# Performance work log

Measured on AMD Instinct MI355X. Metric: run time of the kernel, lower is better.

## Reference

```python
import jax, jax.numpy as jnp
import numpy as np

B, T, D, H = 32, 2048, 256, 256

def setup_inputs() -> dict:
    key = jax.random.key(0)
    ks = jax.random.split(key, 5)
    s = 1.0 / np.sqrt(H)  # PyTorch default uniform scale
    return {
        "x": jax.random.normal(ks[0], (B, T, D), dtype=jnp.float32),
        "W_ih": jax.random.uniform(ks[1], (4 * H, D), jnp.float32, -s, s),
        "W_hh": jax.random.uniform(ks[2], (4 * H, H), jnp.float32, -s, s),
        "b_ih": jax.random.uniform(ks[3], (4 * H,), jnp.float32, -s, s),
        "b_hh": jax.random.uniform(ks[4], (4 * H,), jnp.float32, -s, s),
    }

def reference(x, W_ih, W_hh, b_ih, b_hh):
    # x: [B,T,D]. relu then single-layer LSTM (PyTorch gate order i,f,g,o).
    xr = jax.nn.relu(x)
    # Precompute input contribution to gates: [B,T,4H] -> scan over T as [T,B,4H]
    xg = jnp.einsum("btd,gd->btg", xr, W_ih) + b_ih + b_hh
    xg = jnp.transpose(xg, (1, 0, 2))
    W_hh_T = W_hh.T  # [H,4H]

    def step(carry, xt):
        h, c = carry
        gates = xt + h @ W_hh_T  # [B,4H]
        i, f, g, o = jnp.split(gates, 4, axis=-1)
        i = jax.nn.sigmoid(i)
        f = jax.nn.sigmoid(f)
        g = jnp.tanh(g)
        o = jax.nn.sigmoid(o)
        c = f * c + i * g
        h = o * jnp.tanh(c)
        return (h, c), h

    h0 = jnp.zeros((B, H), dtype=x.dtype)
    c0 = jnp.zeros((B, H), dtype=x.dtype)
    _, ys = jax.lax.scan(step, (h0, c0), xg)  # ys: [T,B,H]
    # dropout p=0.0 (eval) -> identity
    return jnp.transpose(ys, (1, 0, 2))  # [B,T,H]
```

## Files before the change

kernel.cpp:

```cpp
#include <hip/hip_runtime.h>


#define T_STEPS 2048
#define DDIM 256
#define HDIM 256
#define GROUPS 2
#define PARTS 8
#define NBLOCKS (GROUPS * PARTS)
#define NTHREADS 512

typedef __attribute__((ext_vector_type(8))) short short8;
typedef __attribute__((ext_vector_type(4))) float float4_;
typedef __attribute__((ext_vector_type(2))) float float2_;

__device__ inline unsigned short f2bf(float f) {
    unsigned u = __float_as_uint(f);
    return (unsigned short)((u + 0x7fffu + ((u >> 16) & 1u)) >> 16);
}
__device__ inline float sigmoid_f(float x) { return 1.f / (1.f + __expf(-x)); }
__device__ inline float tanh_f(float x) { return 1.f - 2.f / (__expf(2.f * x) + 1.f); }

__global__ __launch_bounds__(NTHREADS, 2)
void lstm_persistent(const float* __restrict__ x,
                     const float* __restrict__ Wih,
                     const float* __restrict__ Whh,
                     const float* __restrict__ bih,
                     const float* __restrict__ bhh,
                     float* __restrict__ out,
                     unsigned int* __restrict__ hbuf,
                     int* __restrict__ flags)
{
    const int tid  = threadIdx.x;
    const int blk  = blockIdx.x;
    const int g    = blk >> 3;
    const int p    = blk & 7;
    const int w    = tid >> 6;
    const int lane = tid & 63;
    const int c16  = lane & 15;
    const int quad = lane >> 4;

    __shared__ float gatesLds[128 * 17];
    __shared__ float biasLds[128];

    if (tid < 128) {
        int n = ((tid >> 5) << 8) + (p << 5) + (tid & 31);
        biasLds[tid] = bih[n] + bhh[n];
    }

    const int r_row = (w << 4) + c16;
    const int wrow  = ((r_row >> 5) << 8) + (p << 5) + (r_row & 31);
    const int k0    = quad << 3;

    short8 wih_f[8], whh_f[8];
#pragma unroll
    for (int kt = 0; kt < 8; ++kt) {
        const float* s1 = Wih + wrow * DDIM + kt * 32 + k0;
        const float* s2 = Whh + wrow * HDIM + kt * 32 + k0;
        short8 v1, v2;
#pragma unroll
        for (int j = 0; j < 8; ++j) { v1[j] = (short)f2bf(s1[j]); v2[j] = (short)f2bf(s2[j]); }
        wih_f[kt] = v1;
        whh_f[kt] = v2;
    }

    const float* xlane = x + (size_t)(g * 16 + c16) * (size_t)(T_STEPS * DDIM);
    float4_ xraw[16];
#pragma unroll
    for (int kt = 0; kt < 8; ++kt) {
        const float* sx = xlane + kt * 32 + k0;
        xraw[2 * kt]     = *(const float4_*)(sx);
        xraw[2 * kt + 1] = *(const float4_*)(sx + 4);
    }

    const int b_e = tid & 15;
    const int up  = (tid >> 4) & 15;
    float c0 = 0.f, c1 = 0.f;

    const int myflag = blk << 4;

    for (int s = 0; s < T_STEPS; ++s) {
        short8 xf[8];
#pragma unroll
        for (int kt = 0; kt < 8; ++kt) {
            short8 v;
#pragma unroll
            for (int j = 0; j < 4; ++j) {
                float a = xraw[2 * kt][j];
                float b = xraw[2 * kt + 1][j];
                v[j]     = (short)f2bf(a > 0.f ? a : 0.f);
                v[j + 4] = (short)f2bf(b > 0.f ? b : 0.f);
            }
            xf[kt] = v;
        }
        float4_ acc0 = {0.f, 0.f, 0.f, 0.f};
        float4_ acc1 = {0.f, 0.f, 0.f, 0.f};
#pragma unroll
        for (int kt = 0; kt < 8; kt += 2) {
            acc0 = __builtin_amdgcn_mfma_f32_16x16x32_bf16(xf[kt],     wih_f[kt],     acc0, 0, 0, 0);
            acc1 = __builtin_amdgcn_mfma_f32_16x16x32_bf16(xf[kt + 1], wih_f[kt + 1], acc1, 0, 0, 0);
        }
        {
            int sn = (s + 1 < T_STEPS) ? s + 1 : s;
            const float* sx = xlane + (size_t)sn * DDIM + k0;
#pragma unroll
            for (int kt = 0; kt < 8; ++kt) {
                xraw[2 * kt]     = *(const float4_*)(sx + kt * 32);
                xraw[2 * kt + 1] = *(const float4_*)(sx + kt * 32 + 4);
            }
        }

        if (tid < PARTS) {
            const int* fp = flags + ((g * PARTS + tid) << 4);
            while (__hip_atomic_load(fp, __ATOMIC_RELAXED, __HIP_MEMORY_SCOPE_AGENT) < s) { }
        }
        __syncthreads();

        const unsigned long long* hq = (const unsigned long long*)
            ((const char*)hbuf + (size_t)(((g * 2 + (s & 1)) * 16 + c16) * 512) + (size_t)(k0 * 2));
        short8 hf[8];
#pragma unroll
        for (int kt = 0; kt < 8; ++kt) {
            unsigned long long q0 = __hip_atomic_load(hq + kt * 8,     __ATOMIC_RELAXED, __HIP_MEMORY_SCOPE_AGENT);
            unsigned long long q1 = __hip_atomic_load(hq + kt * 8 + 1, __ATOMIC_RELAXED, __HIP_MEMORY_SCOPE_AGENT);
            union { unsigned long long q[2]; short8 v; } cvt;
            cvt.q[0] = q0; cvt.q[1] = q1;
            hf[kt] = cvt.v;
        }

#pragma unroll
        for (int kt = 0; kt < 8; kt += 2) {
            acc0 = __builtin_amdgcn_mfma_f32_16x16x32_bf16(hf[kt],     whh_f[kt],     acc0, 0, 0, 0);
            acc1 = __builtin_amdgcn_mfma_f32_16x16x32_bf16(hf[kt + 1], whh_f[kt + 1], acc1, 0, 0, 0);
        }

#pragma unroll
        for (int j = 0; j < 4; ++j)
            gatesLds[r_row * 17 + (quad << 2) + j] = acc0[j] + acc1[j];
        __syncthreads();

        if (tid < 256) {
            const int u0 = up << 1, u1 = (up << 1) + 1;
            float gi0 = gatesLds[u0 * 17 + b_e]         + biasLds[u0];
            float gf0 = gatesLds[(32 + u0) * 17 + b_e]  + biasLds[32 + u0];
            float gg0 = gatesLds[(64 + u0) * 17 + b_e]  + biasLds[64 + u0];
            float go0 = gatesLds[(96 + u0) * 17 + b_e]  + biasLds[96 + u0];
            float gi1 = gatesLds[u1 * 17 + b_e]         + biasLds[u1];
            float gf1 = gatesLds[(32 + u1) * 17 + b_e]  + biasLds[32 + u1];
            float gg1 = gatesLds[(64 + u1) * 17 + b_e]  + biasLds[64 + u1];
            float go1 = gatesLds[(96 + u1) * 17 + b_e]  + biasLds[96 + u1];

            c0 = sigmoid_f(gf0) * c0 + sigmoid_f(gi0) * tanh_f(gg0);
            c1 = sigmoid_f(gf1) * c1 + sigmoid_f(gi1) * tanh_f(gg1);
            float h0 = sigmoid_f(go0) * tanh_f(c0);
            float h1 = sigmoid_f(go1) * tanh_f(c1);

            unsigned hv = (unsigned)f2bf(h0) | ((unsigned)f2bf(h1) << 16);
            unsigned int* hd = hbuf + (((g * 2 + ((s + 1) & 1)) * 16 + b_e) << 7) + (p << 4) + up;
            __hip_atomic_store(hd, hv, __ATOMIC_RELAXED, __HIP_MEMORY_SCOPE_AGENT);

            float2_ ov = {h0, h1};
            *(float2_*)(out + ((size_t)(g * 16 + b_e) * T_STEPS + (size_t)s) * HDIM + (p << 5) + u0) = ov;
        }

        __builtin_amdgcn_s_waitcnt(0);
        __syncthreads();
        if (tid == 0)
            __hip_atomic_store(flags + myflag, s + 1,
                               __ATOMIC_RELAXED, __HIP_MEMORY_SCOPE_AGENT);
    }
}

extern "C" void kernel_launch(void* const* d_in, const int* in_sizes, int n_in,
                              void* d_out, int out_size, void* d_ws, size_t ws_size,
                              hipStream_t stream) {
    (void)in_sizes; (void)n_in; (void)out_size; (void)ws_size;
    const float* x   = (const float*)d_in[0];
    const float* Wih = (const float*)d_in[1];
    const float* Whh = (const float*)d_in[2];
    const float* bih = (const float*)d_in[3];
    const float* bhh = (const float*)d_in[4];
    float* out = (float*)d_out;

    unsigned int* hbuf = (unsigned int*)d_ws;
    int* flags         = (int*)((char*)d_ws + 32768);

    hipMemsetAsync(d_ws, 0, 32768 + NBLOCKS * 64, stream);
    hipLaunchKernelGGL(lstm_persistent, dim3(NBLOCKS), dim3(NTHREADS), 0, stream,
                       x, Wih, Whh, bih, bhh, out, hbuf, flags);
}
```

Baseline: 18.16 ms.

## Replace per-block flag barrier with step-tagged hidden-state words

Each packed bf16 hidden pair now carries the producer's step number in the upper 32 bits of a 64-bit word. Consumers spin directly on the data until every word they read has the expected tag. This removes the separate flag array, the waitcnt, the end-of-step syncthreads and the flag store. The MFMA accumulation is also split across four independent accumulators to shorten dependency chains. The cost is twice the hidden-state traffic, since each read is 64 bits instead of 32, and wavefronts may re-poll many words while they wait.

```diff
diff --git a/kernel.cpp b/kernel.cpp
--- a/kernel.cpp
+++ b/kernel.cpp
@@ -27,8 +27,7 @@
                      const float* __restrict__ bih,
                      const float* __restrict__ bhh,
                      float* __restrict__ out,
-                     unsigned int* __restrict__ hbuf,
-                     int* __restrict__ flags)
+                     unsigned long long* __restrict__ hbuf)
 {
     const int tid  = threadIdx.x;
     const int blk  = blockIdx.x;
@@ -76,8 +75,6 @@
     const int up  = (tid >> 4) & 15;
     float c0 = 0.f, c1 = 0.f;
 
-    const int myflag = blk << 4;
-
     for (int s = 0; s < T_STEPS; ++s) {
         short8 xf[8];
 #pragma unroll
@@ -92,13 +89,13 @@
             }
             xf[kt] = v;
         }
-        float4_ acc0 = {0.f, 0.f, 0.f, 0.f};
-        float4_ acc1 = {0.f, 0.f, 0.f, 0.f};
+        float4_ acc[4];
 #pragma unroll
-        for (int kt = 0; kt < 8; kt += 2) {
-            acc0 = __builtin_amdgcn_mfma_f32_16x16x32_bf16(xf[kt],     wih_f[kt],     acc0, 0, 0, 0);
-            acc1 = __builtin_amdgcn_mfma_f32_16x16x32_bf16(xf[kt + 1], wih_f[kt + 1], acc1, 0, 0, 0);
-        }
+        for (int i = 0; i < 4; ++i) acc[i] = (float4_){0.f, 0.f, 0.f, 0.f};
+#pragma unroll
+        for (int kt = 0; kt < 8; ++kt)
+            acc[kt & 3] = __builtin_amdgcn_mfma_f32_16x16x32_bf16(xf[kt], wih_f[kt], acc[kt & 3], 0, 0, 0);
+
         {
             int sn = (s + 1 < T_STEPS) ? s + 1 : s;
             const float* sx = xlane + (size_t)sn * DDIM + k0;
@@ -109,45 +106,55 @@
             }
         }
 
-        if (tid < PARTS) {
-            const int* fp = flags + ((g * PARTS + tid) << 4);
-            while (__hip_atomic_load(fp, __ATOMIC_RELAXED, __HIP_MEMORY_SCOPE_AGENT) < s) { }
-        }
-        __syncthreads();
-
-        const unsigned long long* hq = (const unsigned long long*)
-            ((const char*)hbuf + (size_t)(((g * 2 + (s & 1)) * 16 + c16) * 512) + (size_t)(k0 * 2));
         short8 hf[8];
+        {
+            const unsigned tag = (unsigned)s;
+            const unsigned long long* hq =
+                hbuf + (size_t)(((g * 2 + (s & 1)) * 16 + c16) * 128 + quad * 4);
+            for (;;) {
+                unsigned long long q[32];
 #pragma unroll
-        for (int kt = 0; kt < 8; ++kt) {
-            unsigned long long q0 = __hip_atomic_load(hq + kt * 8,     __ATOMIC_RELAXED, __HIP_MEMORY_SCOPE_AGENT);
-            unsigned long long q1 = __hip_atomic_load(hq + kt * 8 + 1, __ATOMIC_RELAXED, __HIP_MEMORY_SCOPE_AGENT);
-            union { unsigned long long q[2]; short8 v; } cvt;
-            cvt.q[0] = q0; cvt.q[1] = q1;
-            hf[kt] = cvt.v;
+                for (int kt = 0; kt < 8; ++kt)
+#pragma unroll
+                    for (int i = 0; i < 4; ++i)
+                        q[4 * kt + i] = __hip_atomic_load(hq + kt * 16 + i,
+                                            __ATOMIC_RELAXED, __HIP_MEMORY_SCOPE_AGENT);
+                unsigned chk = 0;
+#pragma unroll
+                for (int i = 0; i < 32; ++i) chk |= (unsigned)(q[i] >> 32) ^ tag;
+                if (!__any(chk != 0)) {
+#pragma unroll
+                    for (int kt = 0; kt < 8; ++kt) {
+                        union { unsigned u[4]; short8 v; } cv;
+#pragma unroll
+                        for (int i = 0; i < 4; ++i) cv.u[i] = (unsigned)q[4 * kt + i];
+                        hf[kt] = cv.v;
+                    }
+                    break;
+                }
+            }
         }
 
 #pragma unroll
-        for (int kt = 0; kt < 8; kt += 2) {
-            acc0 = __builtin_amdgcn_mfma_f32_16x16x32_bf16(hf[kt],     whh_f[kt],     acc0, 0, 0, 0);
-            acc1 = __builtin_amdgcn_mfma_f32_16x16x32_bf16(hf[kt + 1], whh_f[kt + 1], acc1, 0, 0, 0);
-        }
+        for (int kt = 0; kt < 8; ++kt)
+            acc[kt & 3] = __builtin_amdgcn_mfma_f32_16x16x32_bf16(hf[kt], whh_f[kt], acc[kt & 3], 0, 0, 0);
 
 #pragma unroll
         for (int j = 0; j < 4; ++j)
-            gatesLds[r_row * 17 + (quad << 2) + j] = acc0[j] + acc1[j];
+            gatesLds[r_row * 17 + (quad << 2) + j] =
+                (acc[0][j] + acc[1][j]) + (acc[2][j] + acc[3][j]);
         __syncthreads();
 
         if (tid < 256) {
-            const int u0 = up << 1, u1 = (up << 1) + 1;
-            float gi0 = gatesLds[u0 * 17 + b_e]         + biasLds[u0];
-            float gf0 = gatesLds[(32 + u0) * 17 + b_e]  + biasLds[32 + u0];
-            float gg0 = gatesLds[(64 + u0) * 17 + b_e]  + biasLds[64 + u0];
-            float go0 = gatesLds[(96 + u0) * 17 + b_e]  + biasLds[96 + u0];
-            float gi1 = gatesLds[u1 * 17 + b_e]         + biasLds[u1];
-            float gf1 = gatesLds[(32 + u1) * 17 + b_e]  + biasLds[32 + u1];
-            float gg1 = gatesLds[(64 + u1) * 17 + b_e]  + biasLds[64 + u1];
-            float go1 = gatesLds[(96 + u1) * 17 + b_e]  + biasLds[96 + u1];
+            const int u0 = up << 1, u1 = u0 + 1;
+            float gi0 = gatesLds[u0 * 17 + b_e]        + biasLds[u0];
+            float gf0 = gatesLds[(32 + u0) * 17 + b_e] + biasLds[32 + u0];
+            float gg0 = gatesLds[(64 + u0) * 17 + b_e] + biasLds[64 + u0];
+            float go0 = gatesLds[(96 + u0) * 17 + b_e] + biasLds[96 + u0];
+            float gi1 = gatesLds[u1 * 17 + b_e]        + biasLds[u1];
+            float gf1 = gatesLds[(32 + u1) * 17 + b_e] + biasLds[32 + u1];
+            float gg1 = gatesLds[(64 + u1) * 17 + b_e] + biasLds[64 + u1];
+            float go1 = gatesLds[(96 + u1) * 17 + b_e] + biasLds[96 + u1];
 
             c0 = sigmoid_f(gf0) * c0 + sigmoid_f(gi0) * tanh_f(gg0);
             c1 = sigmoid_f(gf1) * c1 + sigmoid_f(gi1) * tanh_f(gg1);
@@ -155,18 +162,15 @@
             float h1 = sigmoid_f(go1) * tanh_f(c1);
 
             unsigned hv = (unsigned)f2bf(h0) | ((unsigned)f2bf(h1) << 16);
-            unsigned int* hd = hbuf + (((g * 2 + ((s + 1) & 1)) * 16 + b_e) << 7) + (p << 4) + up;
-            __hip_atomic_store(hd, hv, __ATOMIC_RELAXED, __HIP_MEMORY_SCOPE_AGENT);
+            unsigned long long word = (unsigned long long)hv
+                                    | ((unsigned long long)(unsigned)(s + 1) << 32);
+            unsigned long long* hd =
+                hbuf + (size_t)(((g * 2 + ((s + 1) & 1)) * 16 + b_e) * 128 + p * 16 + up);
+            __hip_atomic_store(hd, word, __ATOMIC_RELAXED, __HIP_MEMORY_SCOPE_AGENT);
 
             float2_ ov = {h0, h1};
             *(float2_*)(out + ((size_t)(g * 16 + b_e) * T_STEPS + (size_t)s) * HDIM + (p << 5) + u0) = ov;
         }
-
-        __builtin_amdgcn_s_waitcnt(0);
-        __syncthreads();
-        if (tid == 0)
-            __hip_atomic_store(flags + myflag, s + 1,
-                               __ATOMIC_RELAXED, __HIP_MEMORY_SCOPE_AGENT);
     }
 }
 
@@ -181,10 +185,9 @@
     const float* bhh = (const float*)d_in[4];
     float* out = (float*)d_out;
 
-    unsigned int* hbuf = (unsigned int*)d_ws;
-    int* flags         = (int*)((char*)d_ws + 32768);
+    unsigned long long* hbuf = (unsigned long long*)d_ws;
 
-    hipMemsetAsync(d_ws, 0, 32768 + NBLOCKS * 64, stream);
+    hipMemsetAsync(d_ws, 0, 65536, stream);
     hipLaunchKernelGGL(lstm_persistent, dim3(NBLOCKS), dim3(NTHREADS), 0, stream,
-                       x, Wih, Whh, bih, bhh, out, hbuf, flags);
+                       x, Wih, Whh, bih, bhh, out, hbuf);
 }
```

After: 24.27 ms. 33.6% more time.

## Co-locate group blocks on one XCD and use sc0 L2-coherent flag sync

Applied to the files above, without the earlier changes.

The grid grows to 64 blocks and keeps only those whose block index mod 8 is below GROUPS, so that under round-robin XCD dispatch each group's 8 blocks likely share one XCD and its L2. A runtime probe checks this by having the blocks exchange tokens with sc0 loads and stores; if every block sees the tokens within a bound, the group switches to a cheaper protocol. That protocol uses per-wave atomic-add counters, sc0 loads for h, double-buffered gate LDS, and drops the trailing barrier and flag store. The aim is to cut the per-step cross-block synchronization latency that dominates this latency-bound recurrence. The cost is extra idle blocks, a probe at startup, and reliance on a dispatch-placement assumption, with a fallback to the original path when the probe fails.

```diff
diff --git a/kernel.cpp b/kernel.cpp
--- a/kernel.cpp
+++ b/kernel.cpp
@@ -6,12 +6,17 @@
 #define HDIM 256
 #define GROUPS 2
 #define PARTS 8
-#define NBLOCKS (GROUPS * PARTS)
 #define NTHREADS 512
+#define GRID 64
+
+#define PROBE_ROUNDS 6
+#define PROBE_BOUND_FIRST 30000
+#define PROBE_BOUND_LATER 3000
 
 typedef __attribute__((ext_vector_type(8))) short short8;
 typedef __attribute__((ext_vector_type(4))) float float4_;
 typedef __attribute__((ext_vector_type(2))) float float2_;
+typedef __attribute__((ext_vector_type(4))) unsigned uint4_;
 
 __device__ inline unsigned short f2bf(float f) {
     unsigned u = __float_as_uint(f);
@@ -19,6 +24,191 @@
 }
 __device__ inline float sigmoid_f(float x) { return 1.f / (1.f + __expf(-x)); }
 __device__ inline float tanh_f(float x) { return 1.f - 2.f / (__expf(2.f * x) + 1.f); }
+
+__device__ __forceinline__ unsigned ld_u32_sc0(const unsigned* p) {
+    unsigned v;
+    asm volatile("global_load_dword %0, %1, off sc0\n\ts_waitcnt vmcnt(0)"
+                 : "=&v"(v) : "v"(p) : "memory");
+    return v;
+}
+__device__ __forceinline__ void st_u32_sc0(unsigned* p, unsigned v) {
+    asm volatile("global_store_dword %0, %1, off sc0" :: "v"(p), "v"(v) : "memory");
+}
+__device__ __forceinline__ void atomic_add_u32(unsigned* p, unsigned v) {
+    asm volatile("global_atomic_add %0, %1, off" :: "v"(p), "v"(v) : "memory");
+}
+__device__ __forceinline__ unsigned ldmin8_sc0(const unsigned* p) {
+    unsigned a0,a1,a2,a3,a4,a5,a6,a7;
+    asm volatile(
+        "global_load_dword %0, %8, off sc0\n\t"
+        "global_load_dword %1, %8, off offset:64 sc0\n\t"
+        "global_load_dword %2, %8, off offset:128 sc0\n\t"
+        "global_load_dword %3, %8, off offset:192 sc0\n\t"
+        "global_load_dword %4, %8, off offset:256 sc0\n\t"
+        "global_load_dword %5, %8, off offset:320 sc0\n\t"
+        "global_load_dword %6, %8, off offset:384 sc0\n\t"
+        "global_load_dword %7, %8, off offset:448 sc0\n\t"
+        "s_waitcnt vmcnt(0)"
+        : "=&v"(a0), "=&v"(a1), "=&v"(a2), "=&v"(a3),
+          "=&v"(a4), "=&v"(a5), "=&v"(a6), "=&v"(a7)
+        : "v"(p) : "memory");
+    unsigned m = a0 < a1 ? a0 : a1;
+    m = a2 < m ? a2 : m;  m = a3 < m ? a3 : m;
+    m = a4 < m ? a4 : m;  m = a5 < m ? a5 : m;
+    m = a6 < m ? a6 : m;  m = a7 < m ? a7 : m;
+    return m;
+}
+__device__ __forceinline__ void ld_hrow_sc0(const char* p, short8 hf[8]) {
+    uint4_ a0, a1, a2, a3, a4, a5, a6, a7;
+    asm volatile(
+        "global_load_dwordx4 %0, %8, off sc0\n\t"
+        "global_load_dwordx4 %1, %8, off offset:64 sc0\n\t"
+        "global_load_dwordx4 %2, %8, off offset:128 sc0\n\t"
+        "global_load_dwordx4 %3, %8, off offset:192 sc0\n\t"
+        "global_load_dwordx4 %4, %8, off offset:256 sc0\n\t"
+        "global_load_dwordx4 %5, %8, off offset:320 sc0\n\t"
+        "global_load_dwordx4 %6, %8, off offset:384 sc0\n\t"
+        "global_load_dwordx4 %7, %8, off offset:448 sc0\n\t"
+        "s_waitcnt vmcnt(0)"
+        : "=&v"(a0), "=&v"(a1), "=&v"(a2), "=&v"(a3),
+          "=&v"(a4), "=&v"(a5), "=&v"(a6), "=&v"(a7)
+        : "v"(p) : "memory");
+    union { uint4_ u; short8 s; } c;
+    c.u = a0; hf[0] = c.s;  c.u = a1; hf[1] = c.s;
+    c.u = a2; hf[2] = c.s;  c.u = a3; hf[3] = c.s;
+    c.u = a4; hf[4] = c.s;  c.u = a5; hf[5] = c.s;
+    c.u = a6; hf[6] = c.s;  c.u = a7; hf[7] = c.s;
+}
+
+template<bool COLOC>
+__device__ __forceinline__ void lstm_loop(
+    const float* __restrict__ xlane, float* __restrict__ out,
+    char* __restrict__ hbase, unsigned* __restrict__ flags,
+    float (*gatesLds)[128 * 17], const float* biasLds,
+    short8* wih_f, short8* whh_f, float4_* xraw,
+    int g, int p, int tid, int lane, int c16, int quad, int r_row)
+{
+    const int b_e = tid & 15;
+    const int up  = (tid >> 4) & 15;
+    const int k0  = quad << 3;
+    float c0 = 0.f, c1 = 0.f;
+
+    for (int s = 0; s < T_STEPS; ++s) {
+        float* gates = COLOC ? gatesLds[s & 1] : gatesLds[0];
+
+        short8 xf[8];
+#pragma unroll
+        for (int kt = 0; kt < 8; ++kt) {
+            short8 v;
+#pragma unroll
+            for (int j = 0; j < 4; ++j) {
+                float a = xraw[2 * kt][j];
+                float b = xraw[2 * kt + 1][j];
+                v[j]     = (short)f2bf(a > 0.f ? a : 0.f);
+                v[j + 4] = (short)f2bf(b > 0.f ? b : 0.f);
+            }
+            xf[kt] = v;
+        }
+        float4_ acc[4];
+#pragma unroll
+        for (int i = 0; i < 4; ++i) acc[i] = (float4_){0.f, 0.f, 0.f, 0.f};
+#pragma unroll
+        for (int kt = 0; kt < 8; ++kt)
+            acc[kt & 3] = __builtin_amdgcn_mfma_f32_16x16x32_bf16(xf[kt], wih_f[kt], acc[kt & 3], 0, 0, 0);
+
+        {
+            int sn = (s + 1 < T_STEPS) ? s + 1 : s;
+            const float* sx = xlane + (size_t)sn * DDIM + k0;
+#pragma unroll
+            for (int kt = 0; kt < 8; ++kt) {
+                xraw[2 * kt]     = *(const float4_*)(sx + kt * 32);
+                xraw[2 * kt + 1] = *(const float4_*)(sx + kt * 32 + 4);
+            }
+        }
+
+        if (COLOC) {
+            const unsigned thr = 4u * (unsigned)s;
+            if (lane < PARTS) {
+                const unsigned* cp = flags + (size_t)(g * PARTS + lane) * 16;
+                while (ld_u32_sc0(cp) < thr) { }
+            }
+        } else {
+            if (tid < PARTS) {
+                const int* fp = (const int*)(flags + (size_t)(g * PARTS + tid) * 16);
+                while (__hip_atomic_load(fp, __ATOMIC_RELAXED, __HIP_MEMORY_SCOPE_AGENT) < s) { }
+            }
+            __syncthreads();
+        }
+
+        short8 hf[8];
+        const char* hb = hbase + (size_t)(((g * 2 + (s & 1)) * 16 + c16) * 512 + quad * 16);
+        if (COLOC) {
+            ld_hrow_sc0(hb, hf);
+        } else {
+            const unsigned long long* hq = (const unsigned long long*)hb;
+#pragma unroll
+            for (int kt = 0; kt < 8; ++kt) {
+                unsigned long long q0 = __hip_atomic_load(hq + kt * 8,     __ATOMIC_RELAXED, __HIP_MEMORY_SCOPE_AGENT);
+                unsigned long long q1 = __hip_atomic_load(hq + kt * 8 + 1, __ATOMIC_RELAXED, __HIP_MEMORY_SCOPE_AGENT);
+                union { unsigned long long q[2]; short8 v; } cvt;
+                cvt.q[0] = q0; cvt.q[1] = q1;
+                hf[kt] = cvt.v;
+            }
+        }
+
+#pragma unroll
+        for (int kt = 0; kt < 8; ++kt)
+            acc[kt & 3] = __builtin_amdgcn_mfma_f32_16x16x32_bf16(hf[kt], whh_f[kt], acc[kt & 3], 0, 0, 0);
+
+#pragma unroll
+        for (int j = 0; j < 4; ++j)
+            gates[r_row * 17 + (quad << 2) + j] =
+                (acc[0][j] + acc[1][j]) + (acc[2][j] + acc[3][j]);
+        __syncthreads();
+
+        if (tid < 256) {
+            const int u0 = up << 1, u1 = u0 + 1;
+            float gi0 = gates[u0 * 17 + b_e]        + biasLds[u0];
+            float gf0 = gates[(32 + u0) * 17 + b_e] + biasLds[32 + u0];
+            float gg0 = gates[(64 + u0) * 17 + b_e] + biasLds[64 + u0];
+            float go0 = gates[(96 + u0) * 17 + b_e] + biasLds[96 + u0];
+            float gi1 = gates[u1 * 17 + b_e]        + biasLds[u1];
+            float gf1 = gates[(32 + u1) * 17 + b_e] + biasLds[32 + u1];
+            float gg1 = gates[(64 + u1) * 17 + b_e] + biasLds[64 + u1];
+            float go1 = gates[(96 + u1) * 17 + b_e] + biasLds[96 + u1];
+
+            c0 = sigmoid_f(gf0) * c0 + sigmoid_f(gi0) * tanh_f(gg0);
+            c1 = sigmoid_f(gf1) * c1 + sigmoid_f(gi1) * tanh_f(gg1);
+            float h0 = sigmoid_f(go0) * tanh_f(c0);
+            float h1 = sigmoid_f(go1) * tanh_f(c1);
+
+            unsigned hv = (unsigned)f2bf(h0) | ((unsigned)f2bf(h1) << 16);
+            unsigned* hd = (unsigned*)(hbase +
+                (size_t)(((g * 2 + ((s + 1) & 1)) * 16 + b_e) * 512 + (p * 16 + up) * 4));
+
+            if (COLOC) {
+                st_u32_sc0(hd, hv);
+                asm volatile("s_waitcnt vmcnt(0)" ::: "memory");
+                if ((tid & 63) == 0)
+                    atomic_add_u32(flags + (size_t)(g * PARTS + p) * 16, 1u);
+                float2_ ov = {h0, h1};
+                *(float2_*)(out + ((size_t)(g * 16 + b_e) * T_STEPS + (size_t)s) * HDIM + (p << 5) + u0) = ov;
+            } else {
+                __hip_atomic_store(hd, hv, __ATOMIC_RELAXED, __HIP_MEMORY_SCOPE_AGENT);
+                float2_ ov = {h0, h1};
+                *(float2_*)(out + ((size_t)(g * 16 + b_e) * T_STEPS + (size_t)s) * HDIM + (p << 5) + u0) = ov;
+            }
+        }
+
+        if (!COLOC) {
+            __builtin_amdgcn_s_waitcnt(0);
+            __syncthreads();
+            if (tid == 0)
+                __hip_atomic_store((int*)(flags + (size_t)(g * PARTS + p) * 16), s + 1,
+                                   __ATOMIC_RELAXED, __HIP_MEMORY_SCOPE_AGENT);
+        }
+    }
+}
 
 __global__ __launch_bounds__(NTHREADS, 2)
 void lstm_persistent(const float* __restrict__ x,
@@ -27,20 +217,25 @@
                      const float* __restrict__ bih,
                      const float* __restrict__ bhh,
                      float* __restrict__ out,
-                     unsigned int* __restrict__ hbuf,
-                     int* __restrict__ flags)
+                     char* __restrict__ hbase,
+                     unsigned* __restrict__ flags,
+                     unsigned* __restrict__ probe,
+                     unsigned* __restrict__ votes,
+                     unsigned* __restrict__ verdict)
 {
-    const int tid  = threadIdx.x;
-    const int blk  = blockIdx.x;
-    const int g    = blk >> 3;
-    const int p    = blk & 7;
+    const int tid = threadIdx.x;
+    const int blk = blockIdx.x;
+    if ((blk & 7) >= GROUPS) return;
+    const int g = blk & 7;
+    const int p = blk >> 3;
     const int w    = tid >> 6;
     const int lane = tid & 63;
     const int c16  = lane & 15;
     const int quad = lane >> 4;
 
-    __shared__ float gatesLds[128 * 17];
+    __shared__ float gatesLds[2][128 * 17];
     __shared__ float biasLds[128];
+    __shared__ int colocSh;
 
     if (tid < 128) {
         int n = ((tid >> 5) << 8) + (p << 5) + (tid & 31);
@@ -72,102 +267,50 @@
         xraw[2 * kt + 1] = *(const float4_*)(sx + 4);
     }
 
-    const int b_e = tid & 15;
-    const int up  = (tid >> 4) & 15;
-    float c0 = 0.f, c1 = 0.f;
-
-    const int myflag = blk << 4;
-
-    for (int s = 0; s < T_STEPS; ++s) {
-        short8 xf[8];
-#pragma unroll
-        for (int kt = 0; kt < 8; ++kt) {
-            short8 v;
-#pragma unroll
-            for (int j = 0; j < 4; ++j) {
-                float a = xraw[2 * kt][j];
-                float b = xraw[2 * kt + 1][j];
-                v[j]     = (short)f2bf(a > 0.f ? a : 0.f);
-                v[j + 4] = (short)f2bf(b > 0.f ? b : 0.f);
-            }
-            xf[kt] = v;
-        }
-        float4_ acc0 = {0.f, 0.f, 0.f, 0.f};
-        float4_ acc1 = {0.f, 0.f, 0.f, 0.f};
-#pragma unroll
-        for (int kt = 0; kt < 8; kt += 2) {
-            acc0 = __builtin_amdgcn_mfma_f32_16x16x32_bf16(xf[kt],     wih_f[kt],     acc0, 0, 0, 0);
-            acc1 = __builtin_amdgcn_mfma_f32_16x16x32_bf16(xf[kt + 1], wih_f[kt + 1], acc1, 0, 0, 0);
-        }
-        {
-            int sn = (s + 1 < T_STEPS) ? s + 1 : s;
-            const float* sx = xlane + (size_t)sn * DDIM + k0;
-#pragma unroll
-            for (int kt = 0; kt < 8; ++kt) {
-                xraw[2 * kt]     = *(const float4_*)(sx + kt * 32);
-                xraw[2 * kt + 1] = *(const float4_*)(sx + kt * 32 + 4);
-            }
-        }
-
-        if (tid < PARTS) {
-            const int* fp = flags + ((g * PARTS + tid) << 4);
-            while (__hip_atomic_load(fp, __ATOMIC_RELAXED, __HIP_MEMORY_SCOPE_AGENT) < s) { }
-        }
-        __syncthreads();
-
-        const unsigned long long* hq = (const unsigned long long*)
-            ((const char*)hbuf + (size_t)(((g * 2 + (s & 1)) * 16 + c16) * 512) + (size_t)(k0 * 2));
-        short8 hf[8];
-#pragma unroll
-        for (int kt = 0; kt < 8; ++kt) {
-            unsigned long long q0 = __hip_atomic_load(hq + kt * 8,     __ATOMIC_RELAXED, __HIP_MEMORY_SCOPE_AGENT);
-            unsigned long long q1 = __hip_atomic_load(hq + kt * 8 + 1, __ATOMIC_RELAXED, __HIP_MEMORY_SCOPE_AGENT);
-            union { unsigned long long q[2]; short8 v; } cvt;
-            cvt.q[0] = q0; cvt.q[1] = q1;
-            hf[kt] = cvt.v;
-        }
-
-#pragma unroll
-        for (int kt = 0; kt < 8; kt += 2) {
-            acc0 = __builtin_amdgcn_mfma_f32_16x16x32_bf16(hf[kt],     whh_f[kt],     acc0, 0, 0, 0);
-            acc1 = __builtin_amdgcn_mfma_f32_16x16x32_bf16(hf[kt + 1], whh_f[kt + 1], acc1, 0, 0, 0);
-        }
-
-#pragma unroll
-        for (int j = 0; j < 4; ++j)
-            gatesLds[r_row * 17 + (quad << 2) + j] = acc0[j] + acc1[j];
-        __syncthreads();
-
-        if (tid < 256) {
-            const int u0 = up << 1, u1 = (up << 1) + 1;
-            float gi0 = gatesLds[u0 * 17 + b_e]         + biasLds[u0];
-            float gf0 = gatesLds[(32 + u0) * 17 + b_e]  + biasLds[32 + u0];
-            float gg0 = gatesLds[(64 + u0) * 17 + b_e]  + biasLds[64 + u0];
-            float go0 = gatesLds[(96 + u0) * 17 + b_e]  + biasLds[96 + u0];
-            float gi1 = gatesLds[u1 * 17 + b_e]         + biasLds[u1];
-            float gf1 = gatesLds[(32 + u1) * 17 + b_e]  + biasLds[32 + u1];
-            float gg1 = gatesLds[(64 + u1) * 17 + b_e]  + biasLds[64 + u1];
-            float go1 = gatesLds[(96 + u1) * 17 + b_e]  + biasLds[96 + u1];
-
-            c0 = sigmoid_f(gf0) * c0 + sigmoid_f(gi0) * tanh_f(gg0);
-            c1 = sigmoid_f(gf1) * c1 + sigmoid_f(gi1) * tanh_f(gg1);
-            float h0 = sigmoid_f(go0) * tanh_f(c0);
-            float h1 = sigmoid_f(go1) * tanh_f(c1);
-
-            unsigned hv = (unsigned)f2bf(h0) | ((unsigned)f2bf(h1) << 16);
-            unsigned int* hd = hbuf + (((g * 2 + ((s + 1) & 1)) * 16 + b_e) << 7) + (p << 4) + up;
-            __hip_atomic_store(hd, hv, __ATOMIC_RELAXED, __HIP_MEMORY_SCOPE_AGENT);
-
-            float2_ ov = {h0, h1};
-            *(float2_*)(out + ((size_t)(g * 16 + b_e) * T_STEPS + (size_t)s) * HDIM + (p << 5) + u0) = ov;
-        }
-
-        __builtin_amdgcn_s_waitcnt(0);
-        __syncthreads();
-        if (tid == 0)
-            __hip_atomic_store(flags + myflag, s + 1,
+    if (tid == 0) {
+        unsigned myvote = 1u;
+        unsigned* ptok = probe + (size_t)(g * PARTS + p) * 16;
+        const unsigned* pbase = probe + (size_t)(g * PARTS) * 16;
+        for (int r = 1; r <= PROBE_ROUNDS && myvote == 1u; ++r) {
+            st_u32_sc0(ptok, (unsigned)r);
+            asm volatile("s_waitcnt vmcnt(0)" ::: "memory");
+            const int bound = (r == 1) ? PROBE_BOUND_FIRST : PROBE_BOUND_LATER;
+            int ok = 0;
+            for (int it = 0; it < bound; ++it) {
+                if (ldmin8_sc0(pbase) >= (unsigned)r) { ok = 1; break; }
+            }
+            if (!ok) myvote = 2u;
+        }
+        __hip_atomic_store(votes + (size_t)(g * PARTS + p) * 16, myvote,
+                           __ATOMIC_RELAXED, __HIP_MEMORY_SCOPE_AGENT);
+        if (p == 0) {
+            unsigned agg = 1u;
+            for (int i = 0; i < PARTS; ++i) {
+                unsigned v;
+                do {
+                    v = __hip_atomic_load(votes + (size_t)(g * PARTS + i) * 16,
+                                          __ATOMIC_RELAXED, __HIP_MEMORY_SCOPE_AGENT);
+                } while (v == 0u);
+                if (v != 1u) agg = 2u;
+            }
+            __hip_atomic_store(verdict + (size_t)g * 16, agg,
                                __ATOMIC_RELAXED, __HIP_MEMORY_SCOPE_AGENT);
-    }
+        }
+        unsigned fin;
+        do {
+            fin = __hip_atomic_load(verdict + (size_t)g * 16,
+                                    __ATOMIC_RELAXED, __HIP_MEMORY_SCOPE_AGENT);
+        } while (fin == 0u);
+        colocSh = (fin == 1u);
+    }
+    __syncthreads();
+
+    if (colocSh)
+        lstm_loop<true >(xlane, out, hbase, flags, gatesLds, biasLds,
+                         wih_f, whh_f, xraw, g, p, tid, lane, c16, quad, r_row);
+    else
+        lstm_loop<false>(xlane, out, hbase, flags, gatesLds, biasLds,
+                         wih_f, whh_f, xraw, g, p, tid, lane, c16, quad, r_row);
 }
 
 extern "C" void kernel_launch(void* const* d_in, const int* in_sizes, int n_in,
@@ -181,10 +324,13 @@
     const float* bhh = (const float*)d_in[4];
     float* out = (float*)d_out;
 
-    unsigned int* hbuf = (unsigned int*)d_ws;
-    int* flags         = (int*)((char*)d_ws + 32768);
-
-    hipMemsetAsync(d_ws, 0, 32768 + NBLOCKS * 64, stream);
-    hipLaunchKernelGGL(lstm_persistent, dim3(NBLOCKS), dim3(NTHREADS), 0, stream,
-                       x, Wih, Whh, bih, bhh, out, hbuf, flags);
-}
+    char*     hbase   = (char*)d_ws;
+    unsigned* flags   = (unsigned*)((char*)d_ws + 32768);
+    unsigned* probe   = (unsigned*)((char*)d_ws + 33792);
+    unsigned* votes   = (unsigned*)((char*)d_ws + 34816);
+    unsigned* verdict = (unsigned*)((char*)d_ws + 35840);
+
+    hipMemsetAsync(d_ws, 0, 35968, stream);
+    hipLaunchKernelGGL(lstm_persistent, dim3(GRID), dim3(NTHREADS), 0, stream,
+                       x, Wih, Whh, bih, bhh, out, hbase, flags, probe, votes, verdict);
+}
```

New measurement: 20.77 ms. 1.14x slower.

## Split LSTM into a parallel input-GEMM phase and a single-block recurrence

Applied to the files above, without the earlier changes.

Adds a two-phase kernel. In the first phase, 1024 blocks compute the relu(x)·W_ih plus bias gate contributions for all timesteps into a large workspace. In the second phase, two blocks each run the full recurrence for 16 batch rows. Because each block now owns every hidden unit for its rows, the per-step cross-block flag polling and global h exchange are replaced by an LDS double buffer and __syncthreads. W_hh is spread across registers, LDS and a global scratch area that is re-read every step. The new path needs about 268 MB of workspace and otherwise falls back to the old kernel. It also relies on blocks 0 and 1 spinning on a global completion counter while the remaining blocks finish.

```diff
diff --git a/kernel.cpp b/kernel.cpp
--- a/kernel.cpp
+++ b/kernel.cpp
@@ -4,14 +4,21 @@
 #define T_STEPS 2048
 #define DDIM 256
 #define HDIM 256
+#define NTHREADS 512
 #define GROUPS 2
 #define PARTS 8
-#define NBLOCKS (GROUPS * PARTS)
-#define NTHREADS 512
+#define P1_GRID 1024
+#define DONE_TARGET 1024
 
 typedef __attribute__((ext_vector_type(8))) short short8;
 typedef __attribute__((ext_vector_type(4))) float float4_;
 typedef __attribute__((ext_vector_type(2))) float float2_;
+
+#define XG_BYTES   ((size_t)2 * T_STEPS * 64 * 64 * 16)
+#define WSW_OFF    XG_BYTES
+#define WSW_BYTES  ((size_t)2 * 4 * 64 * 64 * 16)
+#define DONE_OFF   (WSW_OFF + WSW_BYTES)
+#define WS_NEED    (DONE_OFF + 64)
 
 __device__ inline unsigned short f2bf(float f) {
     unsigned u = __float_as_uint(f);
@@ -20,15 +27,218 @@
 __device__ inline float sigmoid_f(float x) { return 1.f / (1.f + __expf(-x)); }
 __device__ inline float tanh_f(float x) { return 1.f - 2.f / (__expf(2.f * x) + 1.f); }
 
+
 __global__ __launch_bounds__(NTHREADS, 2)
-void lstm_persistent(const float* __restrict__ x,
-                     const float* __restrict__ Wih,
-                     const float* __restrict__ Whh,
-                     const float* __restrict__ bih,
-                     const float* __restrict__ bhh,
-                     float* __restrict__ out,
-                     unsigned int* __restrict__ hbuf,
-                     int* __restrict__ flags)
+void lstm_twophase(const float* __restrict__ x,
+                   const float* __restrict__ Wih,
+                   const float* __restrict__ Whh,
+                   const float* __restrict__ bih,
+                   const float* __restrict__ bhh,
+                   float* __restrict__ out,
+                   char* __restrict__ ws)
+{
+    float*    xg   = (float*)ws;
+    char*     wsw  = ws + WSW_OFF;
+    unsigned* done = (unsigned*)(ws + DONE_OFF);
+
+    const int tid  = threadIdx.x;
+    const int blk  = blockIdx.x;
+    const int w    = tid >> 6;
+    const int lane = tid & 63;
+    const int c16  = lane & 15;
+    const int quad = lane >> 4;
+
+    __shared__ short8 fragLds[128][64];
+    __shared__ unsigned hLds[2][16][132];
+
+    {
+        const int g     = blk & 1;
+        const int rem   = blk >> 1;
+        const int chunk = rem >> 2;
+        const int nq    = rem & 3;
+        const int nt0   = nq * 16;
+
+        for (int f = w * 16; f < w * 16 + 16; ++f) {
+            const int nt = f >> 3, kt = f & 7;
+            const float* src = Wih + (size_t)((nt0 + nt) * 16 + c16) * DDIM + kt * 32 + quad * 8;
+            short8 v;
+#pragma unroll
+            for (int j = 0; j < 8; ++j) v[j] = (short)f2bf(src[j]);
+            fragLds[f][lane] = v;
+        }
+        __syncthreads();
+
+#pragma unroll 1
+        for (int mi = 0; mi < 2; ++mi) {
+            const int t = chunk * 16 + (w * 2 + mi);
+            const float* xrow = x + ((size_t)(g * 16 + c16) * T_STEPS + t) * DDIM + quad * 8;
+            short8 af[8];
+#pragma unroll
+            for (int kt = 0; kt < 8; ++kt) {
+                short8 v;
+#pragma unroll
+                for (int j = 0; j < 8; ++j) {
+                    float a = xrow[kt * 32 + j];
+                    v[j] = (short)f2bf(a > 0.f ? a : 0.f);
+                }
+                af[kt] = v;
+            }
+#pragma unroll 1
+            for (int ng = 0; ng < 2; ++ng) {
+                float4_ acc[8];
+#pragma unroll
+                for (int i = 0; i < 8; ++i) acc[i] = (float4_){0.f, 0.f, 0.f, 0.f};
+#pragma unroll
+                for (int kt = 0; kt < 8; ++kt)
+#pragma unroll
+                    for (int i = 0; i < 8; ++i)
+                        acc[i] = __builtin_amdgcn_mfma_f32_16x16x32_bf16(
+                            af[kt], fragLds[(ng * 8 + i) * 8 + kt][lane], acc[i], 0, 0, 0);
+#pragma unroll
+                for (int i = 0; i < 8; ++i) {
+                    const int n  = nt0 + ng * 8 + i;
+                    const float bias = bih[n * 16 + c16] + bhh[n * 16 + c16];
+#pragma unroll
+                    for (int j = 0; j < 4; ++j) acc[i][j] += bias;
+                    float4_* dst = (float4_*)xg +
+                        (((size_t)g * T_STEPS + t) * 64 + (n & 7) * 8 + (n >> 3)) * 64 + lane;
+                    *dst = acc[i];
+                }
+            }
+        }
+        __syncthreads();
+        if (tid == 0) {
+            __threadfence();
+            atomicAdd(done, 1u);
+        }
+    }
+
+    if (blk >= 2) return;
+
+    const int g = blk;
+
+    short8 wf[2][8];
+#pragma unroll
+    for (int kt = 0; kt < 2; ++kt)
+#pragma unroll
+        for (int a = 0; a < 8; ++a) {
+            const int n = w + 8 * a;
+            const float* src = Whh + (size_t)(n * 16 + c16) * HDIM + kt * 32 + quad * 8;
+            short8 v;
+#pragma unroll
+            for (int j = 0; j < 8; ++j) v[j] = (short)f2bf(src[j]);
+            wf[kt][a] = v;
+        }
+#pragma unroll
+    for (int kt = 2; kt < 4; ++kt)
+#pragma unroll
+        for (int a = 0; a < 8; ++a) {
+            const int n = w + 8 * a;
+            const float* src = Whh + (size_t)(n * 16 + c16) * HDIM + kt * 32 + quad * 8;
+            short8 v;
+#pragma unroll
+            for (int j = 0; j < 8; ++j) v[j] = (short)f2bf(src[j]);
+            fragLds[(kt - 2) * 64 + n][lane] = v;
+        }
+#pragma unroll
+    for (int kt = 4; kt < 8; ++kt)
+#pragma unroll
+        for (int a = 0; a < 8; ++a) {
+            const int n = w + 8 * a;
+            const float* src = Whh + (size_t)(n * 16 + c16) * HDIM + kt * 32 + quad * 8;
+            short8 v;
+#pragma unroll
+            for (int j = 0; j < 8; ++j) v[j] = (short)f2bf(src[j]);
+            *(short8*)(wsw + ((((size_t)blk * 4 + (kt - 4)) * 64 + n) * 64 + lane) * 16) = v;
+        }
+    for (int i = tid; i < 2 * 16 * 132; i += NTHREADS) ((unsigned*)hLds)[i] = 0u;
+
+    if (tid == 0) {
+        while (__hip_atomic_load(done, __ATOMIC_ACQUIRE, __HIP_MEMORY_SCOPE_AGENT)
+               < DONE_TARGET) { }
+    }
+    __syncthreads();
+
+    const float4_* xg4 = (const float4_*)xg;
+    float4_ xgbuf[8];
+#pragma unroll
+    for (int a = 0; a < 8; ++a)
+        xgbuf[a] = xg4[(((size_t)g * T_STEPS + 0) * 64 + w * 8 + a) * 64 + lane];
+
+    float c_[8];
+#pragma unroll
+    for (int i = 0; i < 8; ++i) c_[i] = 0.f;
+
+    float* outg = out + (size_t)(g * 16) * T_STEPS * HDIM;
+    const char* wswB = wsw + (size_t)blk * 4 * 64 * 64 * 16;
+
+    for (int s = 0; s < T_STEPS; ++s) {
+        float4_ acc[8];
+#pragma unroll
+        for (int a = 0; a < 8; ++a) acc[a] = xgbuf[a];
+        const int sn = (s + 1 < T_STEPS) ? s + 1 : s;
+#pragma unroll
+        for (int a = 0; a < 8; ++a)
+            xgbuf[a] = xg4[(((size_t)g * T_STEPS + sn) * 64 + w * 8 + a) * 64 + lane];
+
+        const char* hbase = (const char*)hLds + (s & 1) * (16 * 132 * 4)
+                          + c16 * 528 + quad * 16;
+
+#pragma unroll
+        for (int kt = 0; kt < 2; ++kt) {
+            const short8 ha = *(const short8*)(hbase + kt * 64);
+#pragma unroll
+            for (int a = 0; a < 8; ++a)
+                acc[a] = __builtin_amdgcn_mfma_f32_16x16x32_bf16(ha, wf[kt][a], acc[a], 0, 0, 0);
+        }
+#pragma unroll
+        for (int kt = 2; kt < 4; ++kt) {
+            const short8 ha = *(const short8*)(hbase + kt * 64);
+#pragma unroll
+            for (int a = 0; a < 8; ++a)
+                acc[a] = __builtin_amdgcn_mfma_f32_16x16x32_bf16(
+                    ha, fragLds[(kt - 2) * 64 + (w + 8 * a)][lane], acc[a], 0, 0, 0);
+        }
+#pragma unroll
+        for (int kt = 4; kt < 8; ++kt) {
+            const short8 ha = *(const short8*)(hbase + kt * 64);
+#pragma unroll
+            for (int a = 0; a < 8; ++a) {
+                const short8 bv = *(const short8*)(wswB +
+                    (((size_t)(kt - 4) * 64 + (w + 8 * a)) * 64 + lane) * 16);
+                acc[a] = __builtin_amdgcn_mfma_f32_16x16x32_bf16(ha, bv, acc[a], 0, 0, 0);
+            }
+        }
+
+        char* hw = (char*)hLds + ((s + 1) & 1) * (16 * 132 * 4);
+#pragma unroll
+        for (int idx = 0; idx < 2; ++idx) {
+            const int u = (w + 8 * idx) * 16 + c16;
+#pragma unroll
+            for (int j = 0; j < 4; ++j) {
+                const float gi = acc[0 + idx][j];
+                const float gf = acc[2 + idx][j];
+                const float gg = acc[4 + idx][j];
+                const float go = acc[6 + idx][j];
+                const float cc = sigmoid_f(gf) * c_[idx * 4 + j]
+                               + sigmoid_f(gi) * tanh_f(gg);
+                c_[idx * 4 + j] = cc;
+                const float h = sigmoid_f(go) * tanh_f(cc);
+                const int b = quad * 4 + j;
+                outg[((size_t)b * T_STEPS + s) * HDIM + u] = h;
+                *(unsigned short*)(hw + b * 528 + u * 2) = f2bf(h);
+            }
+        }
+        __syncthreads();
+    }
+}
+
+
+__global__ __launch_bounds__(NTHREADS, 2)
+void lstm_r2(const float* __restrict__ x, const float* __restrict__ Wih,
+             const float* __restrict__ Whh, const float* __restrict__ bih,
+             const float* __restrict__ bhh, float* __restrict__ out,
+             unsigned int* __restrict__ hbuf, int* __restrict__ flags)
 {
     const int tid  = threadIdx.x;
     const int blk  = blockIdx.x;
@@ -75,7 +285,6 @@
     const int b_e = tid & 15;
     const int up  = (tid >> 4) & 15;
     float c0 = 0.f, c1 = 0.f;
-
     const int myflag = blk << 4;
 
     for (int s = 0; s < T_STEPS; ++s) {
@@ -108,7 +317,6 @@
                 xraw[2 * kt + 1] = *(const float4_*)(sx + kt * 32 + 4);
             }
         }
-
         if (tid < PARTS) {
             const int* fp = flags + ((g * PARTS + tid) << 4);
             while (__hip_atomic_load(fp, __ATOMIC_RELAXED, __HIP_MEMORY_SCOPE_AGENT) < s) { }
@@ -126,13 +334,11 @@
             cvt.q[0] = q0; cvt.q[1] = q1;
             hf[kt] = cvt.v;
         }
-
 #pragma unroll
         for (int kt = 0; kt < 8; kt += 2) {
             acc0 = __builtin_amdgcn_mfma_f32_16x16x32_bf16(hf[kt],     whh_f[kt],     acc0, 0, 0, 0);
             acc1 = __builtin_amdgcn_mfma_f32_16x16x32_bf16(hf[kt + 1], whh_f[kt + 1], acc1, 0, 0, 0);
         }
-
 #pragma unroll
         for (int j = 0; j < 4; ++j)
             gatesLds[r_row * 17 + (quad << 2) + j] = acc0[j] + acc1[j];
@@ -161,7 +367,6 @@
             float2_ ov = {h0, h1};
             *(float2_*)(out + ((size_t)(g * 16 + b_e) * T_STEPS + (size_t)s) * HDIM + (p << 5) + u0) = ov;
         }
-
         __builtin_amdgcn_s_waitcnt(0);
         __syncthreads();
         if (tid == 0)
@@ -173,7 +378,7 @@
 extern "C" void kernel_launch(void* const* d_in, const int* in_sizes, int n_in,
                               void* d_out, int out_size, void* d_ws, size_t ws_size,
                               hipStream_t stream) {
-    (void)in_sizes; (void)n_in; (void)out_size; (void)ws_size;
+    (void)in_sizes; (void)n_in; (void)out_size;
     const float* x   = (const float*)d_in[0];
     const float* Wih = (const float*)d_in[1];
     const float* Whh = (const float*)d_in[2];
@@ -181,10 +386,15 @@
     const float* bhh = (const float*)d_in[4];
     float* out = (float*)d_out;
 
-    unsigned int* hbuf = (unsigned int*)d_ws;
-    int* flags         = (int*)((char*)d_ws + 32768);
-
-    hipMemsetAsync(d_ws, 0, 32768 + NBLOCKS * 64, stream);
-    hipLaunchKernelGGL(lstm_persistent, dim3(NBLOCKS), dim3(NTHREADS), 0, stream,
-                       x, Wih, Whh, bih, bhh, out, hbuf, flags);
+    if (ws_size >= WS_NEED) {
+        hipMemsetAsync((char*)d_ws + DONE_OFF, 0, 64, stream);
+        hipLaunchKernelGGL(lstm_twophase, dim3(P1_GRID), dim3(NTHREADS), 0, stream,
+                           x, Wih, Whh, bih, bhh, out, (char*)d_ws);
+    } else {
+        unsigned int* hbuf = (unsigned int*)d_ws;
+        int* flags         = (int*)((char*)d_ws + 32768);
+        hipMemsetAsync(d_ws, 0, 32768 + 16 * 64, stream);
+        hipLaunchKernelGGL(lstm_r2, dim3(16), dim3(NTHREADS), 0, stream,
+                           x, Wih, Whh, bih, bhh, out, hbuf, flags);
+    }
 }
```

Result: no change. 18.15 ms (-0.0%).
